# Kernel tuning notes

Measured on AMD Instinct MI355X. Metric: run time of the kernel, lower is better.

Reference implementation:

```python
import jax, jax.numpy as jnp
import numpy as np

TAU = 20.0
TH = 1.0
TAU_THETA = 50.0
THETA_INC = 0.5
REFRAC_STEPS = 5
K = 10.0  # surrogate sigmoid sharpness
B, L = 65536, 400


def setup_inputs() -> dict:
    key = jax.random.key(0)
    I = jax.random.normal(key, (B, L), dtype=jnp.float32)
    return {"I": I}


def _lif_forward(I):
    Bn, Ln = I.shape
    dt = I.dtype

    def step(carry, I_t):
        v, theta, ref = carry
        # Euler membrane update: v += -v/tau + I_t
        v = v + (-v / TAU + I_t)
        can_spike = (ref == 0)
        x = v - theta
        s_soft = jax.nn.sigmoid(K * x) * can_spike.astype(dt)
        s_hard = ((x >= 0.0) & can_spike).astype(dt)
        # straight-through: value = s_hard, gradient flows through s_soft
        s = jax.lax.stop_gradient(s_hard - s_soft) + s_soft
        ref = jnp.where(s_hard > 0, jnp.int32(REFRAC_STEPS), jnp.maximum(ref - 1, 0))
        # reset uses detached spike (multiplier is a constant wrt grad)
        v = v * (1.0 - jax.lax.stop_gradient(s))
        # adaptive threshold: decay to base + bump on hard spike
        theta = theta - (theta - TH) / TAU_THETA + THETA_INC * s_hard
        return (v, theta, ref), (s, s_hard)

    init = (jnp.zeros((Bn,), dt), jnp.full((Bn,), TH, dt), jnp.zeros((Bn,), jnp.int32))
    _, (spikes_t, hard_t) = jax.lax.scan(step, init, jnp.swapaxes(I, 0, 1))
    spikes = jnp.swapaxes(spikes_t, 0, 1)       # [B, L]
    hard_spikes = jnp.swapaxes(hard_t, 0, 1)    # [B, L]
    return spikes, hard_spikes


def _soft_lat(spikes):
    Ln = spikes.shape[1]
    time = jnp.arange(Ln, dtype=spikes.dtype)
    w = spikes / (spikes.sum(axis=1, keepdims=True) + 1e-6)
    return (w * time).sum(axis=1)


def reference(I):
    spikes, hard_spikes = _lif_forward(I)
    fired = hard_spikes > 0.5
    has_spike = jnp.any(fired, axis=1)
    first_idx = jnp.argmax(fired, axis=1)
    hard_latency = jnp.where(has_spike, first_idx, I.shape[1]).astype(jnp.int64)
    soft_latency = _soft_lat(spikes)
    return spikes, hard_latency, soft_latency
```

## Files before the change

kernel.cpp:

```cpp
#include <hip/hip_runtime.h>


constexpr int Bsz  = 65536;
constexpr int Lsz  = 400;
constexpr int ROWS = 64;
constexpr int TC   = 40;
constexpr int STRIDE = 41;
constexpr int V4   = TC / 4;

typedef float floatx4 __attribute__((ext_vector_type(4)));

__device__ __forceinline__ int sumpos(unsigned int w) {
    return __popc(w & 0xAAAAAAAAu) + (__popc(w & 0xCCCCCCCCu) << 1) +
           (__popc(w & 0xF0F0F0F0u) << 2) + (__popc(w & 0xFF00FF00u) << 3) +
           (__popc(w & 0xFFFF0000u) << 4);
}

__global__ __launch_bounds__(2 * ROWS)
void lif_kernel(const float* __restrict__ I, float* __restrict__ out)
{
    __shared__ float in2[2][ROWS * STRIDE];
    __shared__ unsigned int bits[2][ROWS * 4];

    const int tid  = threadIdx.x;
    const int wv   = tid >> 6;
    const int lane = tid & 63;
    const int rb   = blockIdx.x * ROWS;

    if (wv == 1) {
        const float* Irow = I + (size_t)(rb + lane) * Lsz;
        float* Sb = out + (size_t)rb * Lsz;
        float4 rg[V4];

        auto issue = [&](int ch) {
#pragma unroll
            for (int it = 0; it < V4; ++it)
                rg[it] = *reinterpret_cast<const float4*>(Irow + ch * TC + it * 4);
        };
        auto put = [&](int buf) {
            const float* f = reinterpret_cast<const float*>(rg);
            float* dst = &in2[buf][lane * STRIDE];
#pragma unroll
            for (int c = 0; c < TC; ++c) dst[c] = f[c];
        };
        auto expand_half = [&](int pair, int half) {
            const unsigned int* bl = bits[pair & 1];
#pragma unroll
            for (int q = 0; q < 10; ++q) {
                const int it  = half * 10 + q;
                const int idx = it * ROWS + lane;
                const int r   = idx / 20;
                const int c4  = idx % 20;
                const unsigned int word = bl[r * 4 + (c4 >> 3)];
                const int bb = (c4 & 7) * 4;
                floatx4 vv = { (float)((word >> (bb + 0)) & 1u),
                               (float)((word >> (bb + 1)) & 1u),
                               (float)((word >> (bb + 2)) & 1u),
                               (float)((word >> (bb + 3)) & 1u) };
                __builtin_nontemporal_store(vv,
                    reinterpret_cast<floatx4*>(Sb + (size_t)r * Lsz + pair * 80 + c4 * 4));
            }
        };

        issue(0); put(0); issue(1);
        __syncthreads();
        for (int pr = 0; pr < 5; ++pr) {
            const int ch = 2 * pr;
            put(1);
            if (ch + 2 < 10) issue(ch + 2);
            if (pr >= 1) expand_half(pr - 1, 0);
            __syncthreads();
            if (ch + 2 < 10) put(0);
            if (ch + 3 < 10) issue(ch + 3);
            if (pr >= 1) expand_half(pr - 1, 1);
            __syncthreads();
        }
        expand_half(4, 0); expand_half(4, 1);
    } else {
        float v = 0.0f, theta = 1.0f;
        int allow = 0, first = Lsz;
        int cnt_i = 0, swt_i = 0;
        unsigned int w0, w1, w2;

        auto scan_chunk = [&](int buf, int t0, int gb) {
            const float* src = &in2[buf][lane * STRIDE];
            float rg[TC];
#pragma unroll
            for (int c = 0; c < TC; ++c) rg[c] = src[c];
#pragma unroll
            for (int c = 0; c < TC; ++c) {
                v = __builtin_fmaf(v, 0.95f, rg[c]);
                const int t = t0 + c;
                const bool hard = (v >= theta) & (t >= allow);
                v     = hard ? 0.0f : v;
                theta = __builtin_fmaf(theta, 0.98f, hard ? 0.52f : 0.02f);
                allow = hard ? (t + 6) : allow;
                const int cg = gb + c;
                const unsigned int m = hard ? (1u << (cg & 31)) : 0u;
                if (cg < 32) w0 |= m; else if (cg < 64) w1 |= m; else w2 |= m;
            }
        };

        __syncthreads();
        for (int pr = 0; pr < 5; ++pr) {
            w0 = w1 = w2 = 0u;
            scan_chunk(0, 2 * pr * TC, 0);
            __syncthreads();
            scan_chunk(1, (2 * pr + 1) * TC, TC);
            const int tp = pr * 80;
            const int p0 = __popc(w0), p1 = __popc(w1), p2 = __popc(w2);
            const int cp = p0 + p1 + p2;
            cnt_i += cp;
            swt_i += tp * cp + sumpos(w0) + sumpos(w1) + 32 * p1 +
                     sumpos(w2) + 64 * p2;
            const int cand = w0 ? tp + (__ffs(w0) - 1)
                           : w1 ? tp + 32 + (__ffs(w1) - 1)
                           : w2 ? tp + 64 + (__ffs(w2) - 1) : Lsz;
            first = min(first, cand);
            *reinterpret_cast<uint4*>(&bits[pr & 1][lane * 4]) =
                make_uint4(w0, w1, w2, 0u);
            __syncthreads();
        }
        const int row = rb + lane;
        out[(size_t)Bsz * Lsz + row]       = (float)first;
        out[(size_t)Bsz * Lsz + Bsz + row] = (float)swt_i / ((float)cnt_i + 1e-6f);
    }
}

extern "C" void kernel_launch(void* const* d_in, const int* in_sizes, int n_in,
                              void* d_out, int out_size, void* d_ws, size_t ws_size,
                              hipStream_t stream)
{
    const float* I = (const float*)d_in[0];
    float* out = (float*)d_out;
    lif_kernel<<<dim3(Bsz / ROWS), dim3(2 * ROWS), 0, stream>>>(I, out);
}
```

Measured before the change: 37.74 us.

## Coalesce input loads across rows and stage 80-step chunks per barrier

The producer wave now loads input with a cooperative row-interleaved float4 pattern, so consecutive lanes read contiguous memory in the same row, instead of each lane streaming its own row. Shared staging now holds full 80-step tiles (stride 81), which halves the number of block barriers per pass. Scalar shared-memory stores in put and doubled register buffers raise LDS bank-conflict and register-pressure risk.

```diff
diff --git a/kernel.cpp b/kernel.cpp
--- a/kernel.cpp
+++ b/kernel.cpp
@@ -1,12 +1,12 @@
 #include <hip/hip_runtime.h>
 
 
-constexpr int Bsz  = 65536;
-constexpr int Lsz  = 400;
-constexpr int ROWS = 64;
-constexpr int TC   = 40;
-constexpr int STRIDE = 41;
-constexpr int V4   = TC / 4;
+constexpr int Bsz   = 65536;
+constexpr int Lsz   = 400;
+constexpr int ROWS  = 64;
+constexpr int PW    = 80;
+constexpr int NPAIR = 5;
+constexpr int STRIDE = 81;
 
 typedef float floatx4 __attribute__((ext_vector_type(4)));
 
@@ -28,68 +28,72 @@
     const int rb   = blockIdx.x * ROWS;
 
     if (wv == 1) {
-        const float* Irow = I + (size_t)(rb + lane) * Lsz;
-        float* Sb = out + (size_t)rb * Lsz;
-        float4 rg[V4];
+        const float* Ib = I   + (size_t)rb * Lsz;
+        float*       Sb = out + (size_t)rb * Lsz;
+        float4 rg[20];
 
-        auto issue = [&](int ch) {
+        auto issue = [&](int p) {
 #pragma unroll
-            for (int it = 0; it < V4; ++it)
-                rg[it] = *reinterpret_cast<const float4*>(Irow + ch * TC + it * 4);
-        };
-        auto put = [&](int buf) {
-            const float* f = reinterpret_cast<const float*>(rg);
-            float* dst = &in2[buf][lane * STRIDE];
-#pragma unroll
-            for (int c = 0; c < TC; ++c) dst[c] = f[c];
-        };
-        auto expand_half = [&](int pair, int half) {
-            const unsigned int* bl = bits[pair & 1];
-#pragma unroll
-            for (int q = 0; q < 10; ++q) {
-                const int it  = half * 10 + q;
-                const int idx = it * ROWS + lane;
+            for (int k = 0; k < 20; ++k) {
+                const int idx = k * 64 + lane;
                 const int r   = idx / 20;
                 const int c4  = idx % 20;
-                const unsigned int word = bl[r * 4 + (c4 >> 3)];
+                rg[k] = *reinterpret_cast<const float4*>(
+                            Ib + (size_t)r * Lsz + p * PW + c4 * 4);
+            }
+        };
+        auto put = [&](float* buf) {
+#pragma unroll
+            for (int k = 0; k < 20; ++k) {
+                const int idx = k * 64 + lane;
+                const int r   = idx / 20;
+                const int c4  = idx % 20;
+                float* d = &buf[r * STRIDE + c4 * 4];
+                d[0] = rg[k].x; d[1] = rg[k].y; d[2] = rg[k].z; d[3] = rg[k].w;
+            }
+        };
+        auto expand = [&](int p) {
+            const unsigned int* bl = bits[p & 1];
+#pragma unroll
+            for (int k = 0; k < 20; ++k) {
+                const int idx = k * 64 + lane;
+                const int r   = idx / 20;
+                const int c4  = idx % 20;
+                const unsigned int w = bl[r * 4 + (c4 >> 3)];
                 const int bb = (c4 & 7) * 4;
-                floatx4 vv = { (float)((word >> (bb + 0)) & 1u),
-                               (float)((word >> (bb + 1)) & 1u),
-                               (float)((word >> (bb + 2)) & 1u),
-                               (float)((word >> (bb + 3)) & 1u) };
+                floatx4 vv = { (float)((w >> (bb + 0)) & 1u),
+                               (float)((w >> (bb + 1)) & 1u),
+                               (float)((w >> (bb + 2)) & 1u),
+                               (float)((w >> (bb + 3)) & 1u) };
                 __builtin_nontemporal_store(vv,
-                    reinterpret_cast<floatx4*>(Sb + (size_t)r * Lsz + pair * 80 + c4 * 4));
+                    reinterpret_cast<floatx4*>(Sb + (size_t)r * Lsz + p * PW + c4 * 4));
             }
         };
 
-        issue(0); put(0); issue(1);
+        issue(0);
+        put(in2[0]);
+        issue(1);
         __syncthreads();
-        for (int pr = 0; pr < 5; ++pr) {
-            const int ch = 2 * pr;
-            put(1);
-            if (ch + 2 < 10) issue(ch + 2);
-            if (pr >= 1) expand_half(pr - 1, 0);
-            __syncthreads();
-            if (ch + 2 < 10) put(0);
-            if (ch + 3 < 10) issue(ch + 3);
-            if (pr >= 1) expand_half(pr - 1, 1);
+        for (int pr = 0; pr < NPAIR; ++pr) {
+            if (pr + 1 < NPAIR) put(in2[(pr + 1) & 1]);
+            if (pr + 2 < NPAIR) issue(pr + 2);
+            if (pr >= 1) expand(pr - 1);
             __syncthreads();
         }
-        expand_half(4, 0); expand_half(4, 1);
+        expand(NPAIR - 1);
     } else {
         float v = 0.0f, theta = 1.0f;
         int allow = 0, first = Lsz;
         int cnt_i = 0, swt_i = 0;
         unsigned int w0, w1, w2;
+        float rgc[40];
 
-        auto scan_chunk = [&](int buf, int t0, int gb) {
-            const float* src = &in2[buf][lane * STRIDE];
-            float rg[TC];
+        auto scan40 = [&](const float* src, int t0, int gb) {
 #pragma unroll
-            for (int c = 0; c < TC; ++c) rg[c] = src[c];
+            for (int c = 0; c < 40; ++c) rgc[c] = src[c];
 #pragma unroll
-            for (int c = 0; c < TC; ++c) {
-                v = __builtin_fmaf(v, 0.95f, rg[c]);
+            for (int c = 0; c < 40; ++c) {
+                v = __builtin_fmaf(v, 0.95f, rgc[c]);
                 const int t = t0 + c;
                 const bool hard = (v >= theta) & (t >= allow);
                 v     = hard ? 0.0f : v;
@@ -102,12 +106,12 @@
         };
 
         __syncthreads();
-        for (int pr = 0; pr < 5; ++pr) {
+        for (int pr = 0; pr < NPAIR; ++pr) {
+            const float* src = &in2[pr & 1][lane * STRIDE];
             w0 = w1 = w2 = 0u;
-            scan_chunk(0, 2 * pr * TC, 0);
-            __syncthreads();
-            scan_chunk(1, (2 * pr + 1) * TC, TC);
-            const int tp = pr * 80;
+            scan40(src,      pr * PW,      0);
+            scan40(src + 40, pr * PW + 40, 40);
+            const int tp = pr * PW;
             const int p0 = __popc(w0), p1 = __popc(w1), p2 = __popc(w2);
             const int cp = p0 + p1 + p2;
             cnt_i += cp;
```

Measured after the change: 43.62 us. 15.6% more time.
